# Kernel tuning notes

Hardware: AMD Instinct MI355X
Metric: run time of the kernel (lower is better)

The kernel has to match this reference:

```python
import jax, jax.numpy as jnp
import numpy as np

B = 8192
L = 64
N = L * L          # 4096 lattice sites
H = 256            # hidden size
NL = 8             # coupling layers
NM = N // 2        # masked sites per layer (checkerboard, even L)


def _checkerboard_indices():
    ii, jj = np.meshgrid(np.arange(L), np.arange(L), indexing='ij')
    cb = ((ii + jj) % 2).reshape(-1)
    out = []
    for parity in (0, 1):
        m = np.where(cb == parity)[0].astype(np.int32)   # frozen sites
        u = np.where(cb != parity)[0].astype(np.int32)   # transformed sites
        out.append((jnp.asarray(m), jnp.asarray(u)))
    return out


def setup_inputs() -> dict:
    key = jax.random.key(0)
    ks = jax.random.split(key, 7)
    sc = 0.02  # keep MLP activations in a sane range (orig zero-inits last layer)
    return {
        'z':  jax.random.normal(ks[0], (B, N), dtype=jnp.float32),
        'W1': jax.random.normal(ks[1], (NL, NM, H), dtype=jnp.float32) * sc,
        'b1': jax.random.normal(ks[2], (NL, H), dtype=jnp.float32) * sc,
        'W2': jax.random.normal(ks[3], (NL, H, H), dtype=jnp.float32) * sc,
        'b2': jax.random.normal(ks[4], (NL, H), dtype=jnp.float32) * sc,
        'W3': jax.random.normal(ks[5], (NL, H, 2 * NM), dtype=jnp.float32) * sc,
        'b3': jax.random.normal(ks[6], (NL, 2 * NM), dtype=jnp.float32) * sc,
    }


def reference(z, W1, b1, W2, b2, W3, b3):
    idx = _checkerboard_indices()  # static constants
    x = z
    log_det = jnp.zeros(z.shape[0], dtype=z.dtype)
    for i in range(NL):
        im, iu = idx[i % 2]
        xm = x[:, im]                                        # (B, NM) gather of frozen half
        h = jax.nn.leaky_relu(xm @ W1[i] + b1[i], 0.2)        # (B, H)
        h = jax.nn.leaky_relu(h @ W2[i] + b2[i], 0.2)         # (B, H)
        st = h @ W3[i] + b3[i]                                # (B, 2*NM)
        s, t = jnp.split(st, 2, axis=1)
        s = 2.0 * jnp.tanh(s)
        x = x.at[:, iu].set(x[:, iu] * jnp.exp(s) + t)        # scatter affine-transformed half
        log_det = log_det + s.sum(axis=1)
    return x, log_det
```

## Files before the change

kernel.cpp:

```cpp
#include <hip/hip_runtime.h>
#include <stdint.h>

#define BATCH   8192
#define NTOT    4096
#define HID     256
#define NLAYERS 8
#define NMASK   2048
#define HALF    ((size_t)BATCH * NMASK)

typedef unsigned short ushort_t;
typedef float  f32x4  __attribute__((ext_vector_type(4)));
typedef __bf16 bf16x8 __attribute__((ext_vector_type(8)));
typedef unsigned short u16x4 __attribute__((ext_vector_type(4)));

__device__ __forceinline__ unsigned short f2bf(float f) {
    union { float f; unsigned u; } v; v.f = f;
    unsigned r = v.u + 0x7FFFu + ((v.u >> 16) & 1u);
    return (unsigned short)(r >> 16);
}
__device__ __forceinline__ float bf2f(unsigned short h) {
    union { float f; unsigned u; } v; v.u = ((unsigned)h) << 16;
    return v.f;
}
__device__ __forceinline__ void split2(float f, unsigned short& hi, unsigned short& lo) {
    hi = f2bf(f);
    lo = f2bf(f - bf2f(hi));
}
__device__ __forceinline__ void async16(const void* g, void* l) {
    __builtin_amdgcn_global_load_lds(
        (const __attribute__((address_space(1))) unsigned int*)g,
        (__attribute__((address_space(3))) unsigned int*)l, 16, 0, 0);
}

__global__ __launch_bounds__(256) void split_transpose_kernel(
    const float* __restrict__ W,
    ushort_t* __restrict__ Whi, ushort_t* __restrict__ Wlo,
    int K, int N)
{
    __shared__ float tile[32][33];
    const int l  = blockIdx.z;
    const int k0 = blockIdx.x * 32;
    const int n0 = blockIdx.y * 32;
    const float* Wl = W + (size_t)l * K * N;
    const int tx = threadIdx.x & 31;
    const int ty = threadIdx.x >> 5;
#pragma unroll
    for (int it = 0; it < 4; ++it) {
        int r = ty + it * 8;
        tile[r][tx] = Wl[(size_t)(k0 + r) * N + (n0 + tx)];
    }
    __syncthreads();
    const size_t obase = (size_t)l * N * K;
#pragma unroll
    for (int it = 0; it < 4; ++it) {
        int r = ty + it * 8;
        float v = tile[tx][r];
        unsigned short hi, lo; split2(v, hi, lo);
        size_t oi = obase + (size_t)(n0 + r) * K + (k0 + tx);
        Whi[oi] = hi; Wlo[oi] = lo;
    }
}

__global__ __launch_bounds__(256) void prep_split(
    const float* __restrict__ z,
    ushort_t* __restrict__ xsh, ushort_t* __restrict__ xsl)
{
    size_t f = (((size_t)blockIdx.x * 256) + threadIdx.x) * 4;
    int row = (int)(f >> 11);
    int n   = (int)(f & 2047);
    int sel = (n >> 5) & 1;
    const float4* zp = (const float4*)(z + (size_t)row * NTOT + 2 * (size_t)n);
    float4 z01 = zp[0], z23 = zp[1];
    float e[8] = {z01.x, z01.y, z01.z, z01.w, z23.x, z23.y, z23.z, z23.w};
    u16x4 ah, al, bh, bl;
#pragma unroll
    for (int i = 0; i < 4; ++i) {
        float c0 = e[2 * i], c1 = e[2 * i + 1];
        float a = sel ? c1 : c0;
        float b = sel ? c0 : c1;
        unsigned short h, l;
        split2(a, h, l); ah[i] = h; al[i] = l;
        split2(b, h, l); bh[i] = h; bl[i] = l;
    }
    size_t off = (size_t)row * NMASK + n;
    *(u16x4*)&xsh[off] = ah;        *(u16x4*)&xsl[off] = al;
    *(u16x4*)&xsh[HALF + off] = bh; *(u16x4*)&xsl[HALF + off] = bl;
}

__global__ __launch_bounds__(256) void finalize_x(
    const ushort_t* __restrict__ xsh, const ushort_t* __restrict__ xsl,
    float* __restrict__ xout)
{
    size_t f = (((size_t)blockIdx.x * 256) + threadIdx.x) * 4;
    int row = (int)(f >> 11);
    int n   = (int)(f & 2047);
    int sel = (n >> 5) & 1;
    size_t off = (size_t)row * NMASK + n;
    u16x4 ah = *(const u16x4*)&xsh[off],        al = *(const u16x4*)&xsl[off];
    u16x4 bh = *(const u16x4*)&xsh[HALF + off], bl = *(const u16x4*)&xsl[HALF + off];
    float o[8];
#pragma unroll
    for (int i = 0; i < 4; ++i) {
        float va = bf2f(ah[i]) + bf2f(al[i]);
        float vb = bf2f(bh[i]) + bf2f(bl[i]);
        o[2 * i]     = sel ? vb : va;
        o[2 * i + 1] = sel ? va : vb;
    }
    float* op = xout + (size_t)row * NTOT + 2 * (size_t)n;
    ((float4*)op)[0] = make_float4(o[0], o[1], o[2], o[3]);
    ((float4*)op)[1] = make_float4(o[4], o[5], o[6], o[7]);
}

__global__ __launch_bounds__(256) void gemm_splitk(
    const ushort_t* __restrict__ Ahi, const ushort_t* __restrict__ Alo, int lda,
    const ushort_t* __restrict__ Bhi, const ushort_t* __restrict__ Blo, int ldb,
    int nk,
    float* __restrict__ Pout)
{
    __shared__ __align__(16) ushort_t Ah[128 * 32], Al[128 * 32];
    __shared__ __align__(16) ushort_t Bh[128 * 32], Bl[128 * 32];

    const int t = threadIdx.x;
    const int row0 = blockIdx.x * 128;
    const int col0 = blockIdx.y * 128;
    const int k0   = blockIdx.z * nk * 32;
    const int w  = t >> 6, L = t & 63;
    const int q  = L >> 4, nl = L & 15;
    const int wr = w >> 1, wc = w & 1;

    f32x4 acc[4][4] = {};

    for (int kt = 0; kt < nk; ++kt) {
        const int kk = k0 + kt * 32;
#pragma unroll
        for (int pass = 0; pass < 2; ++pass) {
            const int chunk = t + pass * 256;
            const int r  = chunk >> 2;
            const int ko = (chunk & 3) * 8;
            async16(Ahi + (size_t)(row0 + r) * lda + kk + ko, (char*)Ah + chunk * 16);
            async16(Alo + (size_t)(row0 + r) * lda + kk + ko, (char*)Al + chunk * 16);
            async16(Bhi + (size_t)(col0 + r) * ldb + kk + ko, (char*)Bh + chunk * 16);
            async16(Blo + (size_t)(col0 + r) * ldb + kk + ko, (char*)Bl + chunk * 16);
        }
        __syncthreads();

        bf16x8 a_h[4], a_l[4];
#pragma unroll
        for (int mt = 0; mt < 4; ++mt) {
            const int r = wr * 64 + mt * 16 + nl;
            a_h[mt] = *(const bf16x8*)&Ah[r * 32 + q * 8];
            a_l[mt] = *(const bf16x8*)&Al[r * 32 + q * 8];
        }
#pragma unroll
        for (int nt = 0; nt < 4; ++nt) {
            const int c = wc * 64 + nt * 16 + nl;
            bf16x8 b_h = *(const bf16x8*)&Bh[c * 32 + q * 8];
            bf16x8 b_l = *(const bf16x8*)&Bl[c * 32 + q * 8];
#pragma unroll
            for (int mt = 0; mt < 4; ++mt) {
                acc[mt][nt] = __builtin_amdgcn_mfma_f32_16x16x32_bf16(b_h, a_h[mt], acc[mt][nt], 0, 0, 0);
                acc[mt][nt] = __builtin_amdgcn_mfma_f32_16x16x32_bf16(b_l, a_h[mt], acc[mt][nt], 0, 0, 0);
                acc[mt][nt] = __builtin_amdgcn_mfma_f32_16x16x32_bf16(b_h, a_l[mt], acc[mt][nt], 0, 0, 0);
            }
        }
        __syncthreads();
    }

    float* out = Pout + (size_t)blockIdx.z * BATCH * HID;
#pragma unroll
    for (int mt = 0; mt < 4; ++mt) {
        const int row = row0 + wr * 64 + mt * 16 + nl;
#pragma unroll
        for (int nt = 0; nt < 4; ++nt) {
            const int col = col0 + wc * 64 + nt * 16 + q * 4;
            *(f32x4*)&out[(size_t)row * HID + col] = acc[mt][nt];
        }
    }
}

__global__ __launch_bounds__(256) void combine_leaky(
    const float* __restrict__ P, int np, const float* __restrict__ bias,
    ushort_t* __restrict__ Ohi, ushort_t* __restrict__ Olo)
{
    size_t f = (((size_t)blockIdx.x * 256) + threadIdx.x) * 4;
    const int col = (int)(f & (HID - 1));
    float4 a = *(const float4*)&P[f];
    for (int j = 1; j < np; ++j) {
        float4 p = *(const float4*)&P[(size_t)j * BATCH * HID + f];
        a.x += p.x; a.y += p.y; a.z += p.z; a.w += p.w;
    }
    float4 bv = *(const float4*)&bias[col];
    float v[4] = {a.x + bv.x, a.y + bv.y, a.z + bv.z, a.w + bv.w};
    u16x4 h, l;
#pragma unroll
    for (int i = 0; i < 4; ++i) {
        float vv = v[i] > 0.f ? v[i] : 0.2f * v[i];
        unsigned short hh, ll; split2(vv, hh, ll);
        h[i] = hh; l[i] = ll;
    }
    *(u16x4*)&Ohi[f] = h;
    *(u16x4*)&Olo[f] = l;
}

__global__ __launch_bounds__(256, 2) void gemm3_update(
    const ushort_t* __restrict__ Ahi, const ushort_t* __restrict__ Alo,
    const ushort_t* __restrict__ Whi, const ushort_t* __restrict__ Wlo,
    const float* __restrict__ b3,
    ushort_t* __restrict__ xsh, ushort_t* __restrict__ xsl,
    float* __restrict__ logdet, int q1)
{
    __shared__ __align__(16) ushort_t Ah[128 * 32], Al[128 * 32];
    __shared__ __align__(16) ushort_t Bsh[128 * 32], Bsl[128 * 32];
    __shared__ __align__(16) ushort_t Bth[128 * 32], Btl[128 * 32];

    const int t = threadIdx.x;
    const int row0 = blockIdx.x * 128;
    const int n0   = blockIdx.y * 128;
    const int w  = t >> 6, L = t & 63;
    const int q  = L >> 4, nl = L & 15;
    const int wr = w >> 1, wc = w & 1;

    f32x4 accS[4][4] = {};
    f32x4 accT[4][4] = {};

    for (int kt = 0; kt < HID / 32; ++kt) {
        const int kk = kt * 32;
#pragma unroll
        for (int pass = 0; pass < 2; ++pass) {
            const int chunk = t + pass * 256;
            const int r  = chunk >> 2;
            const int ko = (chunk & 3) * 8;
            async16(Ahi + (size_t)(row0 + r) * HID + kk + ko, (char*)Ah + chunk * 16);
            async16(Alo + (size_t)(row0 + r) * HID + kk + ko, (char*)Al + chunk * 16);
            const size_t gs = (size_t)(n0 + r) * HID + kk + ko;
            async16(Whi + gs, (char*)Bsh + chunk * 16);
            async16(Wlo + gs, (char*)Bsl + chunk * 16);
            async16(Whi + (size_t)NMASK * HID + gs, (char*)Bth + chunk * 16);
            async16(Wlo + (size_t)NMASK * HID + gs, (char*)Btl + chunk * 16);
        }
        __syncthreads();

        bf16x8 a_h[4], a_l[4];
#pragma unroll
        for (int mt = 0; mt < 4; ++mt) {
            const int r = wr * 64 + mt * 16 + nl;
            a_h[mt] = *(const bf16x8*)&Ah[r * 32 + q * 8];
            a_l[mt] = *(const bf16x8*)&Al[r * 32 + q * 8];
        }
#pragma unroll
        for (int nt = 0; nt < 4; ++nt) {
            const int c = wc * 64 + nt * 16 + nl;
            bf16x8 bs_h = *(const bf16x8*)&Bsh[c * 32 + q * 8];
            bf16x8 bs_l = *(const bf16x8*)&Bsl[c * 32 + q * 8];
            bf16x8 bt_h = *(const bf16x8*)&Bth[c * 32 + q * 8];
            bf16x8 bt_l = *(const bf16x8*)&Btl[c * 32 + q * 8];
#pragma unroll
            for (int mt = 0; mt < 4; ++mt) {
                accS[mt][nt] = __builtin_amdgcn_mfma_f32_16x16x32_bf16(bs_h, a_h[mt], accS[mt][nt], 0, 0, 0);
                accS[mt][nt] = __builtin_amdgcn_mfma_f32_16x16x32_bf16(bs_l, a_h[mt], accS[mt][nt], 0, 0, 0);
                accS[mt][nt] = __builtin_amdgcn_mfma_f32_16x16x32_bf16(bs_h, a_l[mt], accS[mt][nt], 0, 0, 0);
                accT[mt][nt] = __builtin_amdgcn_mfma_f32_16x16x32_bf16(bt_h, a_h[mt], accT[mt][nt], 0, 0, 0);
                accT[mt][nt] = __builtin_amdgcn_mfma_f32_16x16x32_bf16(bt_l, a_h[mt], accT[mt][nt], 0, 0, 0);
                accT[mt][nt] = __builtin_amdgcn_mfma_f32_16x16x32_bf16(bt_h, a_l[mt], accT[mt][nt], 0, 0, 0);
            }
        }
        __syncthreads();
    }

    ushort_t* xh = xsh + (size_t)q1 * HALF;
    ushort_t* xl = xsl + (size_t)q1 * HALF;

    float4 bs4[4], bt4[4];
#pragma unroll
    for (int nt = 0; nt < 4; ++nt) {
        const int n = n0 + wc * 64 + nt * 16 + q * 4;
        bs4[nt] = *(const float4*)&b3[n];
        bt4[nt] = *(const float4*)&b3[n + NMASK];
    }

#pragma unroll
    for (int mt = 0; mt < 4; ++mt) {
        const int row = row0 + wr * 64 + mt * 16 + nl;
        float ldv = 0.f;
#pragma unroll
        for (int nt = 0; nt < 4; ++nt) {
            const int n = n0 + wc * 64 + nt * 16 + q * 4;
            const size_t off = (size_t)row * NMASK + n;
            u16x4 oh = *(const u16x4*)&xh[off];
            u16x4 ol = *(const u16x4*)&xl[off];
            const float* bsp = (const float*)&bs4[nt];
            const float* btp = (const float*)&bt4[nt];
            u16x4 nh, nlo;
#pragma unroll
            for (int r = 0; r < 4; ++r) {
                const float sv = accS[mt][nt][r] + bsp[r];
                const float e2 = __expf(-2.f * fabsf(sv));
                float th = __fdividef(1.f - e2, 1.f + e2);
                th = __builtin_copysignf(th, sv);
                const float s  = 2.f * th;
                const float es = __expf(s);
                const float old = bf2f(oh[r]) + bf2f(ol[r]);
                const float nv  = old * es + accT[mt][nt][r] + btp[r];
                unsigned short hh, ll; split2(nv, hh, ll);
                nh[r] = hh; nlo[r] = ll;
                ldv += s;
            }
            *(u16x4*)&xh[off] = nh;
            *(u16x4*)&xl[off] = nlo;
        }
        ldv += __shfl_xor(ldv, 16);
        ldv += __shfl_xor(ldv, 32);
        if (q == 0)
            atomicAdd(&logdet[row], ldv);
    }
}

extern "C" void kernel_launch(void* const* d_in, const int* in_sizes, int n_in,
                              void* d_out, int out_size, void* d_ws, size_t ws_size,
                              hipStream_t stream)
{
    const float* z  = (const float*)d_in[0];
    const float* W1 = (const float*)d_in[1];
    const float* b1 = (const float*)d_in[2];
    const float* W2 = (const float*)d_in[3];
    const float* b2 = (const float*)d_in[4];
    const float* W3 = (const float*)d_in[5];
    const float* b3 = (const float*)d_in[6];

    float* xout   = (float*)d_out;
    float* logdet = xout + (size_t)BATCH * NTOT;

    ushort_t* ws = (ushort_t*)d_ws;
    size_t o = 0;
    ushort_t* W1h = ws + o; o += (size_t)NLAYERS * HID * NMASK;
    ushort_t* W1l = ws + o; o += (size_t)NLAYERS * HID * NMASK;
    ushort_t* W2h = ws + o; o += (size_t)NLAYERS * HID * HID;
    ushort_t* W2l = ws + o; o += (size_t)NLAYERS * HID * HID;
    ushort_t* W3h = ws + o; o += (size_t)NLAYERS * NTOT * HID;
    ushort_t* W3l = ws + o; o += (size_t)NLAYERS * NTOT * HID;
    ushort_t* h1h = ws + o; o += (size_t)BATCH * HID;
    ushort_t* h1l = ws + o; o += (size_t)BATCH * HID;
    ushort_t* h2h = ws + o; o += (size_t)BATCH * HID;
    ushort_t* h2l = ws + o; o += (size_t)BATCH * HID;
    ushort_t* xsh = ws + o; o += 2 * HALF;
    ushort_t* xsl = ws + o; o += 2 * HALF;
    float*    P   = (float*)(ws + o);

    hipMemsetAsync(logdet, 0, sizeof(float) * BATCH, stream);

    split_transpose_kernel<<<dim3(NMASK / 32, HID / 32, NLAYERS), 256, 0, stream>>>(
        W1, W1h, W1l, NMASK, HID);
    split_transpose_kernel<<<dim3(HID / 32, HID / 32, NLAYERS), 256, 0, stream>>>(
        W2, W2h, W2l, HID, HID);
    split_transpose_kernel<<<dim3(HID / 32, NTOT / 32, NLAYERS), 256, 0, stream>>>(
        W3, W3h, W3l, HID, NTOT);

    prep_split<<<dim3((unsigned)(HALF / 4 / 256)), 256, 0, stream>>>(z, xsh, xsl);

    const unsigned cgrid = (unsigned)((size_t)BATCH * HID / 4 / 256);
    for (int i = 0; i < NLAYERS; ++i) {
        const int p  = i & 1;
        const int q1 = 1 - p;
        gemm_splitk<<<dim3(BATCH / 128, HID / 128, 4), 256, 0, stream>>>(
            xsh + (size_t)p * HALF, xsl + (size_t)p * HALF, NMASK,
            W1h + (size_t)i * HID * NMASK, W1l + (size_t)i * HID * NMASK, NMASK,
            16, P);
        combine_leaky<<<cgrid, 256, 0, stream>>>(P, 4, b1 + (size_t)i * HID, h1h, h1l);
        gemm_splitk<<<dim3(BATCH / 128, HID / 128, 4), 256, 0, stream>>>(
            h1h, h1l, HID,
            W2h + (size_t)i * HID * HID, W2l + (size_t)i * HID * HID, HID,
            2, P);
        combine_leaky<<<cgrid, 256, 0, stream>>>(P, 4, b2 + (size_t)i * HID, h2h, h2l);
        gemm3_update<<<dim3(BATCH / 128, NMASK / 128), 256, 0, stream>>>(
            h2h, h2l,
            W3h + (size_t)i * NTOT * HID, W3l + (size_t)i * NTOT * HID,
            b3 + (size_t)i * NTOT,
            xsh, xsl, logdet, q1);
    }

    finalize_x<<<dim3((unsigned)(HALF / 4 / 256)), 256, 0, stream>>>(xsh, xsl, xout);
}
```

Before: 1.501 ms.

## Swizzle LDS tiles, raise occupancy hints, and widen split-K for first GEMM

Applies an XOR swizzle to the 16-byte chunk positions in the shared-memory A/B tiles of both GEMM kernels, so the MFMA fragment reads spread across LDS banks instead of conflicting. Raises the launch-bounds occupancy hints (gemm_splitk to 4 blocks, gemm3_update to 3). Uses 8-way split-K for the first-layer GEMM when the workspace is large enough, which doubles partial-sum traffic through combine_leaky. Higher occupancy hints may force register spills in the larger gemm3 kernel.

```diff
diff --git a/kernel.cpp b/kernel.cpp
--- a/kernel.cpp
+++ b/kernel.cpp
@@ -111,7 +111,7 @@
     ((float4*)op)[1] = make_float4(o[4], o[5], o[6], o[7]);
 }
 
-__global__ __launch_bounds__(256) void gemm_splitk(
+__global__ __launch_bounds__(256, 4) void gemm_splitk(
     const ushort_t* __restrict__ Ahi, const ushort_t* __restrict__ Alo, int lda,
     const ushort_t* __restrict__ Bhi, const ushort_t* __restrict__ Blo, int ldb,
     int nk,
@@ -136,7 +136,8 @@
         for (int pass = 0; pass < 2; ++pass) {
             const int chunk = t + pass * 256;
             const int r  = chunk >> 2;
-            const int ko = (chunk & 3) * 8;
+            const int j  = chunk & 3;
+            const int ko = (j ^ ((r >> 1) & 3)) * 8;
             async16(Ahi + (size_t)(row0 + r) * lda + kk + ko, (char*)Ah + chunk * 16);
             async16(Alo + (size_t)(row0 + r) * lda + kk + ko, (char*)Al + chunk * 16);
             async16(Bhi + (size_t)(col0 + r) * ldb + kk + ko, (char*)Bh + chunk * 16);
@@ -148,14 +149,16 @@
 #pragma unroll
         for (int mt = 0; mt < 4; ++mt) {
             const int r = wr * 64 + mt * 16 + nl;
-            a_h[mt] = *(const bf16x8*)&Ah[r * 32 + q * 8];
-            a_l[mt] = *(const bf16x8*)&Al[r * 32 + q * 8];
+            const int sl = q ^ ((r >> 1) & 3);
+            a_h[mt] = *(const bf16x8*)&Ah[r * 32 + sl * 8];
+            a_l[mt] = *(const bf16x8*)&Al[r * 32 + sl * 8];
         }
 #pragma unroll
         for (int nt = 0; nt < 4; ++nt) {
             const int c = wc * 64 + nt * 16 + nl;
-            bf16x8 b_h = *(const bf16x8*)&Bh[c * 32 + q * 8];
-            bf16x8 b_l = *(const bf16x8*)&Bl[c * 32 + q * 8];
+            const int sl = q ^ ((c >> 1) & 3);
+            bf16x8 b_h = *(const bf16x8*)&Bh[c * 32 + sl * 8];
+            bf16x8 b_l = *(const bf16x8*)&Bl[c * 32 + sl * 8];
 #pragma unroll
             for (int mt = 0; mt < 4; ++mt) {
                 acc[mt][nt] = __builtin_amdgcn_mfma_f32_16x16x32_bf16(b_h, a_h[mt], acc[mt][nt], 0, 0, 0);
@@ -202,7 +205,7 @@
     *(u16x4*)&Olo[f] = l;
 }
 
-__global__ __launch_bounds__(256, 2) void gemm3_update(
+__global__ __launch_bounds__(256, 3) void gemm3_update(
     const ushort_t* __restrict__ Ahi, const ushort_t* __restrict__ Alo,
     const ushort_t* __restrict__ Whi, const ushort_t* __restrict__ Wlo,
     const float* __restrict__ b3,
@@ -229,7 +232,8 @@
         for (int pass = 0; pass < 2; ++pass) {
             const int chunk = t + pass * 256;
             const int r  = chunk >> 2;
-            const int ko = (chunk & 3) * 8;
+            const int j  = chunk & 3;
+            const int ko = (j ^ ((r >> 1) & 3)) * 8;
             async16(Ahi + (size_t)(row0 + r) * HID + kk + ko, (char*)Ah + chunk * 16);
             async16(Alo + (size_t)(row0 + r) * HID + kk + ko, (char*)Al + chunk * 16);
             const size_t gs = (size_t)(n0 + r) * HID + kk + ko;
@@ -244,16 +248,18 @@
 #pragma unroll
         for (int mt = 0; mt < 4; ++mt) {
             const int r = wr * 64 + mt * 16 + nl;
-            a_h[mt] = *(const bf16x8*)&Ah[r * 32 + q * 8];
-            a_l[mt] = *(const bf16x8*)&Al[r * 32 + q * 8];
+            const int sl = q ^ ((r >> 1) & 3);
+            a_h[mt] = *(const bf16x8*)&Ah[r * 32 + sl * 8];
+            a_l[mt] = *(const bf16x8*)&Al[r * 32 + sl * 8];
         }
 #pragma unroll
         for (int nt = 0; nt < 4; ++nt) {
             const int c = wc * 64 + nt * 16 + nl;
-            bf16x8 bs_h = *(const bf16x8*)&Bsh[c * 32 + q * 8];
-            bf16x8 bs_l = *(const bf16x8*)&Bsl[c * 32 + q * 8];
-            bf16x8 bt_h = *(const bf16x8*)&Bth[c * 32 + q * 8];
-            bf16x8 bt_l = *(const bf16x8*)&Btl[c * 32 + q * 8];
+            const int sl = q ^ ((c >> 1) & 3);
+            bf16x8 bs_h = *(const bf16x8*)&Bsh[c * 32 + sl * 8];
+            bf16x8 bs_l = *(const bf16x8*)&Bsl[c * 32 + sl * 8];
+            bf16x8 bt_h = *(const bf16x8*)&Bth[c * 32 + sl * 8];
+            bf16x8 bt_l = *(const bf16x8*)&Btl[c * 32 + sl * 8];
 #pragma unroll
             for (int mt = 0; mt < 4; ++mt) {
                 accS[mt][nt] = __builtin_amdgcn_mfma_f32_16x16x32_bf16(bs_h, a_h[mt], accS[mt][nt], 0, 0, 0);
@@ -346,6 +352,11 @@
     ushort_t* xsl = ws + o; o += 2 * HALF;
     float*    P   = (float*)(ws + o);
 
+    const size_t p_off_bytes = o * sizeof(ushort_t);
+    const size_t p8_bytes = (size_t)8 * BATCH * HID * sizeof(float);
+    const int np1 = (ws_size >= p_off_bytes + p8_bytes) ? 8 : 4;
+    const int nk1 = 64 / np1;
+
     hipMemsetAsync(logdet, 0, sizeof(float) * BATCH, stream);
 
     split_transpose_kernel<<<dim3(NMASK / 32, HID / 32, NLAYERS), 256, 0, stream>>>(
@@ -361,11 +372,11 @@
     for (int i = 0; i < NLAYERS; ++i) {
         const int p  = i & 1;
         const int q1 = 1 - p;
-        gemm_splitk<<<dim3(BATCH / 128, HID / 128, 4), 256, 0, stream>>>(
+        gemm_splitk<<<dim3(BATCH / 128, HID / 128, np1), 256, 0, stream>>>(
             xsh + (size_t)p * HALF, xsl + (size_t)p * HALF, NMASK,
             W1h + (size_t)i * HID * NMASK, W1l + (size_t)i * HID * NMASK, NMASK,
-            16, P);
-        combine_leaky<<<cgrid, 256, 0, stream>>>(P, 4, b1 + (size_t)i * HID, h1h, h1l);
+            nk1, P);
+        combine_leaky<<<cgrid, 256, 0, stream>>>(P, np1, b1 + (size_t)i * HID, h1h, h1l);
         gemm_splitk<<<dim3(BATCH / 128, HID / 128, 4), 256, 0, stream>>>(
             h1h, h1l, HID,
             W2h + (size_t)i * HID * HID, W2l + (size_t)i * HID * HID, HID,
```

Result: slower. 2.246 ms (+49.6%).
